# Performance work log

Hardware: AMD Instinct MI355X
Metric: run time of the kernel (lower is better)

Reference implementation:

```python
import jax, jax.numpy as jnp
import numpy as np

K_CORR = 2048        # num_correspondences (init kwarg)
MAX_CORR = 8192      # static pad size for the variable-length nonzero output
THRES_START = 0.5
THRES_STEP = 0.01


def setup_inputs() -> dict:
    key = jax.random.key(0)
    k1, k2, k3 = jax.random.split(key, 3)
    N = M = 8193  # 8192 superpoints + 1 dustbin
    # shift so exp(scores) is mostly well below the 0.5 starting threshold,
    # making the iterative threshold search actually iterate (as in practice
    # with log-domain OT scores)
    matching_scores = jax.random.normal(k1, (N, M), dtype=jnp.float32) - 5.0
    ref_n2p_scores_c = jax.random.uniform(k2, (N - 1,), dtype=jnp.float32)
    src_n2p_scores_c = jax.random.uniform(k3, (M - 1,), dtype=jnp.float32)
    return {
        "matching_scores": matching_scores,
        "ref_n2p_scores_c": ref_n2p_scores_c,
        "src_n2p_scores_c": src_n2p_scores_c,
    }


def _find_thres(inner, k):
    """Replicates: while count(score[:-1,:-1] > thres) < k: thres -= 0.01."""
    def cond(t):
        return jnp.sum(inner > t) < k
    def body(t):
        return t - jnp.float32(THRES_STEP)
    return jax.lax.while_loop(cond, body, jnp.float32(THRES_START))


def reference(matching_scores, ref_n2p_scores_c, src_n2p_scores_c):
    s = jnp.exp(matching_scores)
    # n2p reweighting of the non-dustbin block, as in the torch in-place update
    inner = s[:-1, :-1] * (ref_n2p_scores_c[:, None] * src_n2p_scores_c[None, :])
    # threshold search is discrete -> not differentiated
    thres = _find_thres(jax.lax.stop_gradient(inner), K_CORR)
    mask = inner > thres
    count = jnp.sum(mask)
    # torch returns variable-length nonzero in row-major order; we pad to MAX_CORR
    r, c = jnp.nonzero(mask, size=MAX_CORR, fill_value=0)
    valid = jnp.arange(MAX_CORR) < count
    corr_scores = jnp.where(valid, inner[r, c], 0.0)
    ref_corr_indices = jnp.where(valid, r, -1)
    src_corr_indices = jnp.where(valid, c, -1)
    return ref_corr_indices, src_corr_indices, corr_scores
```

## Files before the change

kernel.cpp:

```cpp
#include <hip/hip_runtime.h>

#define NROWS 8192
#define NCOLS 8192
#define LD    8193
#define NBINS 64
#define KCORR 2048
#define MAXC  8192
#define FCUT_LOG (-2.5257286443082556f)

__device__ __forceinline__ float inner_val(float m, float rr, float sc) {
    float p = rr * sc;
    return expf(m) * p;
}

__global__ void init_kernel(float* __restrict__ out, unsigned* __restrict__ hist) {
    int i = blockIdx.x * blockDim.x + threadIdx.x;
    if (i < 2 * MAXC)       out[i] = -1.0f;
    else if (i < 3 * MAXC)  out[i] = 0.0f;
    if (i < NBINS) hist[i] = 0u;
}

__device__ __forceinline__ void slow_bin(float m, float rr, float sc,
                                         const float* t, unsigned* sub) {
    float v = inner_val(m, rr, sc);
    int g = (int)floorf((0.5f - v) * 100.0f) + 1;
    g = (g < 0) ? 0 : ((g > NBINS) ? NBINS : g);
    while (g < NBINS && t[g] >= v) ++g;
    while (g > 0 && t[g - 1] < v) --g;
    atomicAdd(&sub[g], 1u);
}

__global__ __launch_bounds__(256) void hist_kernel(
    const float* __restrict__ ms, const float* __restrict__ refs,
    const float* __restrict__ srcs, unsigned* __restrict__ hist,
    unsigned* __restrict__ rowhistT, int use_rowhist)
{
    __shared__ float t[NBINS];
    __shared__ unsigned sub[NBINS];
    int tid = threadIdx.x;
    if (tid == 0) {
        float tv = 0.5f;
        for (int n = 0; n < NBINS; ++n) { t[n] = tv; tv = tv - 0.01f; }
    }
    if (tid < NBINS) sub[tid] = 0u;
    __syncthreads();

    int row = blockIdx.x;
    float rr = refs[row];
    const float* mrow = ms + (size_t)row * LD;

    int s = (4 - (row & 3)) & 3;
    if (tid < s) {
        float m = mrow[tid];
        if (m > FCUT_LOG) slow_bin(m, rr, srcs[tid], t, sub);
    }
    const float4* b4 = (const float4*)(mrow + s);
    int nb = (NCOLS - s) >> 2;

    float4 q[8];
    #pragma unroll
    for (int k = 0; k < 8; ++k) {
        int i = tid + 256 * k;
        if (k < 7 || i < nb) q[k] = b4[i];
        else q[k] = make_float4(-1e30f, -1e30f, -1e30f, -1e30f);
    }
    #pragma unroll
    for (int k = 0; k < 8; ++k) {
        int c0 = s + 4 * (tid + 256 * k);
        if (q[k].x > FCUT_LOG) slow_bin(q[k].x, rr, srcs[c0 + 0], t, sub);
        if (q[k].y > FCUT_LOG) slow_bin(q[k].y, rr, srcs[c0 + 1], t, sub);
        if (q[k].z > FCUT_LOG) slow_bin(q[k].z, rr, srcs[c0 + 2], t, sub);
        if (q[k].w > FCUT_LOG) slow_bin(q[k].w, rr, srcs[c0 + 3], t, sub);
    }
    int done = s + (nb << 2);
    if (tid < NCOLS - done) {
        int c = done + tid;
        float m = mrow[c];
        if (m > FCUT_LOG) slow_bin(m, rr, srcs[c], t, sub);
    }
    __syncthreads();

    if (tid < 64) {
        unsigned v = sub[tid];
        unsigned p = v;
        #pragma unroll
        for (int off = 1; off < 64; off <<= 1) {
            unsigned u = __shfl_up(p, off);
            if (tid >= off) p += u;
        }
        unsigned slowtot = __shfl(p, 63);
        if (use_rowhist)
            rowhistT[(size_t)tid * NROWS + row] = (tid == 63) ? (unsigned)NCOLS : p;
        unsigned g = (tid == 63) ? (v + (unsigned)NCOLS - slowtot) : v;
        if (g) atomicAdd(&hist[tid], g);
    }
}

__global__ __launch_bounds__(1024) void mid_kernel(
    const unsigned* __restrict__ hist, const unsigned* __restrict__ rowhistT,
    float* __restrict__ thres, unsigned* __restrict__ nstar,
    unsigned* __restrict__ rowoff, int use_rowhist)
{
    __shared__ int s_ns;
    __shared__ unsigned ssum[1024];
    int tid = threadIdx.x;
    if (tid < 64) {
        unsigned h = hist[tid];
        unsigned cum = h;
        #pragma unroll
        for (int off = 1; off < 64; off <<= 1) {
            unsigned u = __shfl_up(cum, off);
            if (tid >= off) cum += u;
        }
        unsigned long long mk = __ballot(cum >= (unsigned)KCORR);
        int nsel = mk ? (int)(__ffsll((unsigned long long)mk) - 1) : (NBINS - 1);
        if (tid == 0) {
            float tv = 0.5f;
            for (int n = 0; n < nsel; ++n) tv = tv - 0.01f;
            *thres = tv;
            *nstar = (unsigned)nsel;
            s_ns = nsel;
        }
    }
    __syncthreads();
    if (!use_rowhist) return;
    int ns = s_ns;
    const unsigned* rc = rowhistT + (size_t)ns * NROWS;
    int r0 = tid * 8;
    unsigned c[8], s = 0;
    #pragma unroll
    for (int k = 0; k < 8; ++k) { c[k] = rc[r0 + k]; s += c[k]; }
    ssum[tid] = s;
    __syncthreads();
    for (int off = 1; off < 1024; off <<= 1) {
        unsigned v = (tid >= off) ? ssum[tid - off] : 0u;
        __syncthreads();
        ssum[tid] += v;
        __syncthreads();
    }
    unsigned excl = ssum[tid] - s;
    #pragma unroll
    for (int k = 0; k < 8; ++k) { rowoff[r0 + k] = excl; excl += c[k]; }
    if (tid == 1023) rowoff[NROWS] = excl;
}

__global__ __launch_bounds__(256) void count_kernel(
    const float* __restrict__ ms, const float* __restrict__ refs,
    const float* __restrict__ srcs, const float* __restrict__ thresp,
    unsigned* __restrict__ rowcnt)
{
    __shared__ unsigned tot;
    if (threadIdx.x == 0) tot = 0;
    __syncthreads();
    int row = blockIdx.x;
    float rr = refs[row];
    float th = *thresp;
    const float* mrow = ms + (size_t)row * LD;
    unsigned cnt = 0;
    for (int c = threadIdx.x; c < NCOLS; c += 256)
        cnt += (inner_val(mrow[c], rr, srcs[c]) > th) ? 1u : 0u;
    atomicAdd(&tot, cnt);
    __syncthreads();
    if (threadIdx.x == 0) rowcnt[row] = tot;
}

__global__ __launch_bounds__(1024) void scan_kernel(
    const unsigned* __restrict__ rowcnt, unsigned* __restrict__ rowoff)
{
    __shared__ unsigned ssum[1024];
    int tid = threadIdx.x;
    int r0 = tid * 8;
    unsigned c[8], s = 0;
    for (int k = 0; k < 8; ++k) { c[k] = rowcnt[r0 + k]; s += c[k]; }
    ssum[tid] = s;
    __syncthreads();
    for (int off = 1; off < 1024; off <<= 1) {
        unsigned v = (tid >= off) ? ssum[tid - off] : 0u;
        __syncthreads();
        ssum[tid] += v;
        __syncthreads();
    }
    unsigned excl = ssum[tid] - s;
    for (int k = 0; k < 8; ++k) { rowoff[r0 + k] = excl; excl += c[k]; }
    if (tid == 1023) rowoff[NROWS] = excl;
}

__global__ __launch_bounds__(256) void write_kernel(
    const float* __restrict__ ms, const float* __restrict__ refs,
    const float* __restrict__ srcs, const float* __restrict__ thresp,
    const unsigned* __restrict__ nstar, const unsigned* __restrict__ rowoff,
    float* __restrict__ out)
{
    __shared__ float s_src[NCOLS];
    __shared__ unsigned s_active;
    int tid = threadIdx.x;
    int wave = tid >> 6, lane = tid & 63;
    int row = blockIdx.x * 4 + wave;
    unsigned base = rowoff[row], next = rowoff[row + 1];
    bool act = (base != next) && (base < MAXC);
    if (tid == 0) s_active = 0u;
    __syncthreads();
    if (act && lane == 0) atomicOr(&s_active, 1u);
    __syncthreads();
    if (!s_active) return;
    for (int i = tid; i < NCOLS / 4; i += 256)
        ((float4*)s_src)[i] = ((const float4*)srcs)[i];
    __syncthreads();
    if (!act) return;

    float th = *thresp;
    bool fastok = (*nstar <= 41u);
    float rr = refs[row];
    const float* mrow = ms + (size_t)row * LD;
    int s = (4 - (row & 3)) & 3;
    float* outR = out;
    float* outC = out + MAXC;
    float* outS = out + 2 * MAXC;
    unsigned running = base;

    if (s) {
        bool pred = false; float v = 0.f;
        if (lane < s) {
            float m = mrow[lane];
            if (!fastok || m > FCUT_LOG) { v = inner_val(m, rr, s_src[lane]); pred = v > th; }
        }
        unsigned long long mk = __ballot(pred);
        if (pred) {
            unsigned pos = running + (unsigned)__popcll(mk & ((1ull << lane) - 1ull));
            if (pos < MAXC) { outR[pos] = (float)row; outC[pos] = (float)lane; outS[pos] = v; }
        }
        running += (unsigned)__popcll(mk);
    }

    const float4* b4 = (const float4*)(mrow + s);
    int nb = (NCOLS - s) >> 2;
    for (int i0 = 0; i0 < nb && running < next && running < MAXC; i0 += 256) {
        float4 q[4];
        #pragma unroll
        for (int k = 0; k < 4; ++k) {
            int i = i0 + 64 * k + lane;
            q[k] = (i < nb) ? b4[i] : make_float4(-1e30f, -1e30f, -1e30f, -1e30f);
        }
        #pragma unroll
        for (int k = 0; k < 4; ++k) {
            int i = i0 + 64 * k + lane;
            int c0 = s + 4 * i;
            float mm[4] = {q[k].x, q[k].y, q[k].z, q[k].w};
            float vv[4]; int pr[4]; unsigned cnt = 0;
            #pragma unroll
            for (int j = 0; j < 4; ++j) {
                pr[j] = 0; vv[j] = 0.f;
                if (i < nb && (!fastok || mm[j] > FCUT_LOG)) {
                    vv[j] = inner_val(mm[j], rr, s_src[c0 + j]);
                    pr[j] = vv[j] > th;
                }
                cnt += (unsigned)pr[j];
            }
            unsigned inc = cnt;
            #pragma unroll
            for (int off = 1; off < 64; off <<= 1) {
                unsigned u = __shfl_up(inc, off);
                if (lane >= off) inc += u;
            }
            unsigned tot = __shfl(inc, 63);
            unsigned pos = running + inc - cnt;
            #pragma unroll
            for (int j = 0; j < 4; ++j) {
                if (pr[j]) {
                    if (pos < MAXC) {
                        outR[pos] = (float)row;
                        outC[pos] = (float)(c0 + j);
                        outS[pos] = vv[j];
                    }
                    ++pos;
                }
            }
            running += tot;
            if (running >= next || running >= MAXC) break;
        }
    }
}

extern "C" void kernel_launch(void* const* d_in, const int* in_sizes, int n_in,
                              void* d_out, int out_size, void* d_ws, size_t ws_size,
                              hipStream_t stream) {
    const float* ms  = (const float*)d_in[0];
    const float* ref = (const float*)d_in[1];
    const float* src = (const float*)d_in[2];
    float* out = (float*)d_out;

    char* w = (char*)d_ws;
    unsigned* hist   = (unsigned*)(w);
    float*    thres  = (float*)(w + 256);
    unsigned* nstar  = (unsigned*)(w + 260);
    unsigned* rowcnt = (unsigned*)(w + 512);
    unsigned* rowoff = (unsigned*)(w + 512 + NROWS * 4);
    size_t rh_off = 512 + (size_t)NROWS * 4 + (size_t)(NROWS + 1) * 4;
    rh_off = (rh_off + 255) & ~(size_t)255;
    unsigned* rowhistT = (unsigned*)(w + rh_off);
    int use_rowhist = (ws_size >= rh_off + (size_t)NROWS * NBINS * 4) ? 1 : 0;

    init_kernel<<<96, 256, 0, stream>>>(out, hist);
    hist_kernel<<<NROWS, 256, 0, stream>>>(ms, ref, src, hist, rowhistT, use_rowhist);
    mid_kernel<<<1, 1024, 0, stream>>>(hist, rowhistT, thres, nstar, rowoff, use_rowhist);
    if (!use_rowhist) {
        count_kernel<<<NROWS, 256, 0, stream>>>(ms, ref, src, thres, rowcnt);
        scan_kernel<<<1, 1024, 0, stream>>>(rowcnt, rowoff);
    }
    write_kernel<<<NROWS / 4, 256, 0, stream>>>(ms, ref, src, thres, nstar, rowoff, out);
}
```

Measured before the change: 429.8 us.

## Cache per-row candidate columns in histogram pass to avoid rereading matrix in write

The histogram kernel now records the columns and values of entries above the log cutoff into a per-row candidate buffer in workspace. The write kernel compacts these candidates with a ballot and ranks them by column, so it no longer rescans the full matrix row. Rows with too many candidates or hits fall back to a plain full-row scan. It also adds count and scan kernels that exit early unless the threshold bin falls in a fallback range. The cost is extra shared atomics and global stores in the histogram pass, plus two more kernel launches.

```diff
diff --git a/kernel.cpp b/kernel.cpp
--- a/kernel.cpp
+++ b/kernel.cpp
@@ -6,6 +6,7 @@
 #define NBINS 64
 #define KCORR 2048
 #define MAXC  8192
+#define CAP   192
 #define FCUT_LOG (-2.5257286443082556f)
 
 __device__ __forceinline__ float inner_val(float m, float rr, float sc) {
@@ -13,34 +14,46 @@
     return expf(m) * p;
 }
 
-__global__ void init_kernel(float* __restrict__ out, unsigned* __restrict__ hist) {
+__global__ void init_kernel(float* __restrict__ out, unsigned* __restrict__ hist,
+                            unsigned* __restrict__ candcnt) {
     int i = blockIdx.x * blockDim.x + threadIdx.x;
     if (i < 2 * MAXC)       out[i] = -1.0f;
     else if (i < 3 * MAXC)  out[i] = 0.0f;
     if (i < NBINS) hist[i] = 0u;
-}
-
-__device__ __forceinline__ void slow_bin(float m, float rr, float sc,
-                                         const float* t, unsigned* sub) {
+    if (i < NROWS) candcnt[i] = 0u;
+}
+
+__device__ __forceinline__ void slow_bin(float m, float rr, float sc, int col,
+                                         const float* t, unsigned* sub,
+                                         unsigned* s_cnt, unsigned* ccol,
+                                         float* cval, int use_cand) {
     float v = inner_val(m, rr, sc);
     int g = (int)floorf((0.5f - v) * 100.0f) + 1;
     g = (g < 0) ? 0 : ((g > NBINS) ? NBINS : g);
     while (g < NBINS && t[g] >= v) ++g;
     while (g > 0 && t[g - 1] < v) --g;
     atomicAdd(&sub[g], 1u);
+    if (use_cand) {
+        unsigned slot = atomicAdd(s_cnt, 1u);
+        if (slot < CAP) { ccol[slot] = (unsigned)col; cval[slot] = v; }
+    }
 }
 
 __global__ __launch_bounds__(256) void hist_kernel(
     const float* __restrict__ ms, const float* __restrict__ refs,
     const float* __restrict__ srcs, unsigned* __restrict__ hist,
-    unsigned* __restrict__ rowhistT, int use_rowhist)
+    unsigned* __restrict__ rowhistT, int use_rowhist,
+    unsigned* __restrict__ candcnt, unsigned* __restrict__ cand_col,
+    float* __restrict__ cand_v, int use_cand)
 {
     __shared__ float t[NBINS];
     __shared__ unsigned sub[NBINS];
+    __shared__ unsigned s_cnt;
     int tid = threadIdx.x;
     if (tid == 0) {
         float tv = 0.5f;
         for (int n = 0; n < NBINS; ++n) { t[n] = tv; tv = tv - 0.01f; }
+        s_cnt = 0u;
     }
     if (tid < NBINS) sub[tid] = 0u;
     __syncthreads();
@@ -48,11 +61,14 @@
     int row = blockIdx.x;
     float rr = refs[row];
     const float* mrow = ms + (size_t)row * LD;
+    unsigned* ccol = cand_col + (size_t)row * CAP;
+    float*    cval = cand_v  + (size_t)row * CAP;
 
     int s = (4 - (row & 3)) & 3;
     if (tid < s) {
         float m = mrow[tid];
-        if (m > FCUT_LOG) slow_bin(m, rr, srcs[tid], t, sub);
+        if (m > FCUT_LOG)
+            slow_bin(m, rr, srcs[tid], tid, t, sub, &s_cnt, ccol, cval, use_cand);
     }
     const float4* b4 = (const float4*)(mrow + s);
     int nb = (NCOLS - s) >> 2;
@@ -67,16 +83,21 @@
     #pragma unroll
     for (int k = 0; k < 8; ++k) {
         int c0 = s + 4 * (tid + 256 * k);
-        if (q[k].x > FCUT_LOG) slow_bin(q[k].x, rr, srcs[c0 + 0], t, sub);
-        if (q[k].y > FCUT_LOG) slow_bin(q[k].y, rr, srcs[c0 + 1], t, sub);
-        if (q[k].z > FCUT_LOG) slow_bin(q[k].z, rr, srcs[c0 + 2], t, sub);
-        if (q[k].w > FCUT_LOG) slow_bin(q[k].w, rr, srcs[c0 + 3], t, sub);
+        bool any = (q[k].x > FCUT_LOG) | (q[k].y > FCUT_LOG) |
+                   (q[k].z > FCUT_LOG) | (q[k].w > FCUT_LOG);
+        if (any) {
+            if (q[k].x > FCUT_LOG) slow_bin(q[k].x, rr, srcs[c0 + 0], c0 + 0, t, sub, &s_cnt, ccol, cval, use_cand);
+            if (q[k].y > FCUT_LOG) slow_bin(q[k].y, rr, srcs[c0 + 1], c0 + 1, t, sub, &s_cnt, ccol, cval, use_cand);
+            if (q[k].z > FCUT_LOG) slow_bin(q[k].z, rr, srcs[c0 + 2], c0 + 2, t, sub, &s_cnt, ccol, cval, use_cand);
+            if (q[k].w > FCUT_LOG) slow_bin(q[k].w, rr, srcs[c0 + 3], c0 + 3, t, sub, &s_cnt, ccol, cval, use_cand);
+        }
     }
     int done = s + (nb << 2);
     if (tid < NCOLS - done) {
         int c = done + tid;
         float m = mrow[c];
-        if (m > FCUT_LOG) slow_bin(m, rr, srcs[c], t, sub);
+        if (m > FCUT_LOG)
+            slow_bin(m, rr, srcs[c], c, t, sub, &s_cnt, ccol, cval, use_cand);
     }
     __syncthreads();
 
@@ -93,6 +114,8 @@
             rowhistT[(size_t)tid * NROWS + row] = (tid == 63) ? (unsigned)NCOLS : p;
         unsigned g = (tid == 63) ? (v + (unsigned)NCOLS - slowtot) : v;
         if (g) atomicAdd(&hist[tid], g);
+    } else if (tid == 64 && use_cand) {
+        candcnt[row] = s_cnt;
     }
 }
 
@@ -144,29 +167,38 @@
     if (tid == 1023) rowoff[NROWS] = excl;
 }
 
-__global__ __launch_bounds__(256) void count_kernel(
+__global__ __launch_bounds__(256) void count2_kernel(
     const float* __restrict__ ms, const float* __restrict__ refs,
     const float* __restrict__ srcs, const float* __restrict__ thresp,
-    unsigned* __restrict__ rowcnt)
-{
+    const unsigned* __restrict__ nstar, unsigned* __restrict__ rowcnt,
+    int use_rowhist)
+{
+    int ns = (int)*nstar;
+    if (use_rowhist && !(ns >= 42 && ns < 63)) return;
     __shared__ unsigned tot;
-    if (threadIdx.x == 0) tot = 0;
-    __syncthreads();
-    int row = blockIdx.x;
-    float rr = refs[row];
     float th = *thresp;
-    const float* mrow = ms + (size_t)row * LD;
-    unsigned cnt = 0;
-    for (int c = threadIdx.x; c < NCOLS; c += 256)
-        cnt += (inner_val(mrow[c], rr, srcs[c]) > th) ? 1u : 0u;
-    atomicAdd(&tot, cnt);
-    __syncthreads();
-    if (threadIdx.x == 0) rowcnt[row] = tot;
-}
-
-__global__ __launch_bounds__(1024) void scan_kernel(
-    const unsigned* __restrict__ rowcnt, unsigned* __restrict__ rowoff)
-{
+    for (int r4 = 0; r4 < 4; ++r4) {
+        int row = blockIdx.x * 4 + r4;
+        if (threadIdx.x == 0) tot = 0;
+        __syncthreads();
+        float rr = refs[row];
+        const float* mrow = ms + (size_t)row * LD;
+        unsigned cnt = 0;
+        for (int c = threadIdx.x; c < NCOLS; c += 256)
+            cnt += (inner_val(mrow[c], rr, srcs[c]) > th) ? 1u : 0u;
+        atomicAdd(&tot, cnt);
+        __syncthreads();
+        if (threadIdx.x == 0) rowcnt[row] = tot;
+        __syncthreads();
+    }
+}
+
+__global__ __launch_bounds__(1024) void scan2_kernel(
+    const unsigned* __restrict__ rowcnt, const unsigned* __restrict__ nstar,
+    unsigned* __restrict__ rowoff, int use_rowhist)
+{
+    int ns = (int)*nstar;
+    if (use_rowhist && !(ns >= 42 && ns < 63)) return;
     __shared__ unsigned ssum[1024];
     int tid = threadIdx.x;
     int r0 = tid * 8;
@@ -185,99 +217,77 @@
     if (tid == 1023) rowoff[NROWS] = excl;
 }
 
-__global__ __launch_bounds__(256) void write_kernel(
+__global__ __launch_bounds__(256) void cwrite_kernel(
     const float* __restrict__ ms, const float* __restrict__ refs,
     const float* __restrict__ srcs, const float* __restrict__ thresp,
     const unsigned* __restrict__ nstar, const unsigned* __restrict__ rowoff,
-    float* __restrict__ out)
-{
-    __shared__ float s_src[NCOLS];
-    __shared__ unsigned s_active;
-    int tid = threadIdx.x;
-    int wave = tid >> 6, lane = tid & 63;
-    int row = blockIdx.x * 4 + wave;
+    const unsigned* __restrict__ candcnt, const unsigned* __restrict__ cand_col,
+    const float* __restrict__ cand_v, float* __restrict__ out, int use_cand)
+{
+    __shared__ unsigned s_col[4][64];
+    __shared__ float    s_val[4][64];
+    int tid = threadIdx.x, wv = tid >> 6, lane = tid & 63;
+    int row = blockIdx.x * 4 + wv;
     unsigned base = rowoff[row], next = rowoff[row + 1];
-    bool act = (base != next) && (base < MAXC);
-    if (tid == 0) s_active = 0u;
-    __syncthreads();
-    if (act && lane == 0) atomicOr(&s_active, 1u);
-    __syncthreads();
-    if (!s_active) return;
-    for (int i = tid; i < NCOLS / 4; i += 256)
-        ((float4*)s_src)[i] = ((const float4*)srcs)[i];
-    __syncthreads();
-    if (!act) return;
-
+    if (base == next || base >= MAXC) return;
     float th = *thresp;
-    bool fastok = (*nstar <= 41u);
+    int ns = (int)*nstar;
+    unsigned k = next - base;
+    bool full = (!use_cand) || (ns >= 42) || (candcnt[row] > CAP) || (k > 64);
+
+    if (!full) {
+        unsigned C = candcnt[row];
+        const unsigned* cc = cand_col + (size_t)row * CAP;
+        const float*    cv = cand_v  + (size_t)row * CAP;
+        unsigned nrun = 0;
+        for (unsigned c0 = 0; c0 < C; c0 += 64) {
+            unsigned i = c0 + lane;
+            bool sel = false; unsigned col = 0; float v = 0.f;
+            if (i < C) { col = cc[i]; v = cv[i]; sel = (v > th); }
+            unsigned long long mk = __ballot(sel);
+            if (sel) {
+                unsigned idx = nrun + (unsigned)__popcll(mk & ((1ull << lane) - 1ull));
+                if (idx < 64) { s_col[wv][idx] = col; s_val[wv][idx] = v; }
+            }
+            nrun += (unsigned)__popcll(mk);
+        }
+        __builtin_amdgcn_s_waitcnt(0);
+        __builtin_amdgcn_wave_barrier();
+        unsigned kk = (nrun < k) ? nrun : k;
+        if (kk > 64) kk = 64;
+        if (lane < (int)kk) {
+            unsigned mycol = s_col[wv][lane];
+            float    myval = s_val[wv][lane];
+            unsigned rank = 0;
+            for (unsigned j = 0; j < kk; ++j)
+                rank += (s_col[wv][j] < mycol) ? 1u : 0u;
+            unsigned pos = base + rank;
+            if (pos < MAXC) {
+                out[pos]            = (float)row;
+                out[MAXC + pos]     = (float)mycol;
+                out[2 * MAXC + pos] = myval;
+            }
+        }
+        return;
+    }
+
     float rr = refs[row];
     const float* mrow = ms + (size_t)row * LD;
-    int s = (4 - (row & 3)) & 3;
-    float* outR = out;
-    float* outC = out + MAXC;
-    float* outS = out + 2 * MAXC;
     unsigned running = base;
-
-    if (s) {
-        bool pred = false; float v = 0.f;
-        if (lane < s) {
-            float m = mrow[lane];
-            if (!fastok || m > FCUT_LOG) { v = inner_val(m, rr, s_src[lane]); pred = v > th; }
-        }
+    for (int c0 = 0; c0 < NCOLS && running < next && running < MAXC; c0 += 64) {
+        int col = c0 + lane;
+        float v = inner_val(mrow[col], rr, srcs[col]);
+        bool pred = v > th;
         unsigned long long mk = __ballot(pred);
         if (pred) {
             unsigned pos = running + (unsigned)__popcll(mk & ((1ull << lane) - 1ull));
-            if (pos < MAXC) { outR[pos] = (float)row; outC[pos] = (float)lane; outS[pos] = v; }
+            if (pos < MAXC) {
+                out[pos]            = (float)row;
+                out[MAXC + pos]     = (float)col;
+                out[2 * MAXC + pos] = v;
+            }
         }
         running += (unsigned)__popcll(mk);
-    }
-
-    const float4* b4 = (const float4*)(mrow + s);
-    int nb = (NCOLS - s) >> 2;
-    for (int i0 = 0; i0 < nb && running < next && running < MAXC; i0 += 256) {
-        float4 q[4];
-        #pragma unroll
-        for (int k = 0; k < 4; ++k) {
-            int i = i0 + 64 * k + lane;
-            q[k] = (i < nb) ? b4[i] : make_float4(-1e30f, -1e30f, -1e30f, -1e30f);
-        }
-        #pragma unroll
-        for (int k = 0; k < 4; ++k) {
-            int i = i0 + 64 * k + lane;
-            int c0 = s + 4 * i;
-            float mm[4] = {q[k].x, q[k].y, q[k].z, q[k].w};
-            float vv[4]; int pr[4]; unsigned cnt = 0;
-            #pragma unroll
-            for (int j = 0; j < 4; ++j) {
-                pr[j] = 0; vv[j] = 0.f;
-                if (i < nb && (!fastok || mm[j] > FCUT_LOG)) {
-                    vv[j] = inner_val(mm[j], rr, s_src[c0 + j]);
-                    pr[j] = vv[j] > th;
-                }
-                cnt += (unsigned)pr[j];
-            }
-            unsigned inc = cnt;
-            #pragma unroll
-            for (int off = 1; off < 64; off <<= 1) {
-                unsigned u = __shfl_up(inc, off);
-                if (lane >= off) inc += u;
-            }
-            unsigned tot = __shfl(inc, 63);
-            unsigned pos = running + inc - cnt;
-            #pragma unroll
-            for (int j = 0; j < 4; ++j) {
-                if (pr[j]) {
-                    if (pos < MAXC) {
-                        outR[pos] = (float)row;
-                        outC[pos] = (float)(c0 + j);
-                        outS[pos] = vv[j];
-                    }
-                    ++pos;
-                }
-            }
-            running += tot;
-            if (running >= next || running >= MAXC) break;
-        }
     }
 }
 
@@ -298,14 +308,27 @@
     size_t rh_off = 512 + (size_t)NROWS * 4 + (size_t)(NROWS + 1) * 4;
     rh_off = (rh_off + 255) & ~(size_t)255;
     unsigned* rowhistT = (unsigned*)(w + rh_off);
-    int use_rowhist = (ws_size >= rh_off + (size_t)NROWS * NBINS * 4) ? 1 : 0;
-
-    init_kernel<<<96, 256, 0, stream>>>(out, hist);
-    hist_kernel<<<NROWS, 256, 0, stream>>>(ms, ref, src, hist, rowhistT, use_rowhist);
-    mid_kernel<<<1, 1024, 0, stream>>>(hist, rowhistT, thres, nstar, rowoff, use_rowhist);
-    if (!use_rowhist) {
-        count_kernel<<<NROWS, 256, 0, stream>>>(ms, ref, src, thres, rowcnt);
-        scan_kernel<<<1, 1024, 0, stream>>>(rowcnt, rowoff);
-    }
-    write_kernel<<<NROWS / 4, 256, 0, stream>>>(ms, ref, src, thres, nstar, rowoff, out);
-}
+    size_t cc_off = rh_off + (size_t)NBINS * NROWS * 4;
+    unsigned* candcnt  = (unsigned*)(w + cc_off);
+    size_t col_off = cc_off + (size_t)NROWS * 4;
+    unsigned* cand_col = (unsigned*)(w + col_off);
+    size_t cv_off = col_off + (size_t)NROWS * CAP * 4;
+    float* cand_v      = (float*)(w + cv_off);
+    size_t end_off = cv_off + (size_t)NROWS * CAP * 4;
+
+    int use_rowhist = (ws_size >= cc_off) ? 1 : 0;
+    int use_cand    = (ws_size >= end_off) ? 1 : 0;
+
+    init_kernel<<<96, 256, 0, stream>>>(out, hist, candcnt);
+    hist_kernel<<<NROWS, 256, 0, stream>>>(ms, ref, src, hist, rowhistT,
+                                           use_rowhist, candcnt, cand_col,
+                                           cand_v, use_cand);
+    mid_kernel<<<1, 1024, 0, stream>>>(hist, rowhistT, thres, nstar, rowoff,
+                                       use_rowhist);
+    count2_kernel<<<NROWS / 4, 256, 0, stream>>>(ms, ref, src, thres, nstar,
+                                                 rowcnt, use_rowhist);
+    scan2_kernel<<<1, 1024, 0, stream>>>(rowcnt, nstar, rowoff, use_rowhist);
+    cwrite_kernel<<<NROWS / 4, 256, 0, stream>>>(ms, ref, src, thres, nstar,
+                                                 rowoff, candcnt, cand_col,
+                                                 cand_v, out, use_cand);
+}
```

New measurement: 410.3 us. -4.5%, faster.
